# Kernel tuning notes

Measured on AMD Instinct MI355X. Metric: run time of the kernel, lower is better.

Reference implementation:

```python
import jax, jax.numpy as jnp
import numpy as np

BOARD_H, BOARD_W = 10, 9
NUM_NODES = BOARD_H * BOARD_W  # 90
NUM_HEADS = 4


def _build_base_adjacency():
    adj = np.zeros((NUM_NODES, NUM_NODES), dtype=np.float32)
    for y in range(BOARD_H):
        for x in range(BOARD_W):
            idx = y * BOARD_W + x
            for dy, dx in [(0, 1), (0, -1), (1, 0), (-1, 0)]:
                ny, nx = y + dy, x + dx
                if 0 <= ny < BOARD_H and 0 <= nx < BOARD_W:
                    adj[idx, ny * BOARD_W + nx] = 1.0
            for nx in range(BOARD_W):
                if nx != x and abs(nx - x) <= 4:
                    nidx = y * BOARD_W + nx
                    adj[idx, nidx] = max(adj[idx, nidx], 1.0 / abs(nx - x))
            for ny in range(BOARD_H):
                if ny != y and abs(ny - y) <= 5:
                    nidx = ny * BOARD_W + x
                    adj[idx, nidx] = max(adj[idx, nidx], 1.0 / abs(ny - y))
            adj[idx, idx] = 1.0
    deg = np.clip(adj.sum(-1, keepdims=True), 1.0, None)
    return adj / deg  # (90, 90)


def _pos_encoding():
    px = (np.arange(BOARD_W, dtype=np.float32) / BOARD_W)
    py = (np.arange(BOARD_H, dtype=np.float32) / BOARD_H)
    gx = np.broadcast_to(px[None, :], (BOARD_H, BOARD_W)).reshape(-1)
    gy = np.broadcast_to(py[:, None], (BOARD_H, BOARD_W)).reshape(-1)
    return np.stack([gx, gy], axis=-1)  # (90, 2)


def _gat_layer(x, adj, W, a_src, a_dst, gamma, beta):
    B, N, _ = x.shape
    h = (x @ W).reshape(B, N, NUM_HEADS, -1)          # (B,N,H,D)
    s_src = jnp.einsum('bnhd,hd->bhn', h, a_src)       # (B,H,N)
    s_dst = jnp.einsum('bnhd,hd->bhn', h, a_dst)
    attn = s_src[..., :, None] + s_dst[..., None, :]   # (B,H,N,N)
    attn = jax.nn.leaky_relu(attn, 0.2)
    attn = jnp.where((adj == 0)[None, None], -jnp.inf, attn)
    attn = jax.nn.softmax(attn, axis=-1)
    attn = jnp.nan_to_num(attn, nan=0.0)
    out = jnp.einsum('bhij,bjhd->bihd', attn, h).reshape(B * N, -1)
    # BatchNorm1d in training mode: biased batch stats over (B*N)
    mean = out.mean(0)
    var = out.var(0)
    out = (out - mean) * jax.lax.rsqrt(var + 1e-5) * gamma + beta
    return jax.nn.relu(out.reshape(B, N, -1))


def setup_inputs() -> dict:
    key = jax.random.key(0)
    ks = jax.random.split(key, 16)
    B, F_in, Hd, Dout = 2048, 16, 64, 128
    hdim = Hd // NUM_HEADS
    p = lambda k, s: (jax.random.normal(k, s, dtype=jnp.float32) * 0.1)
    return {
        'board_planes': jax.random.uniform(ks[0], (B, 14, BOARD_H, BOARD_W), dtype=jnp.float32),
        'in_W': p(ks[1], (F_in, Hd)), 'in_b': p(ks[2], (Hd,)),
        'W0': p(ks[3], (Hd, Hd)), 'asrc0': p(ks[4], (NUM_HEADS, hdim)), 'adst0': p(ks[5], (NUM_HEADS, hdim)),
        'g0': jnp.ones((Hd,), jnp.float32), 'b0': jnp.zeros((Hd,), jnp.float32),
        'W1': p(ks[6], (Hd, Hd)), 'asrc1': p(ks[7], (NUM_HEADS, hdim)), 'adst1': p(ks[8], (NUM_HEADS, hdim)),
        'g1': jnp.ones((Hd,), jnp.float32), 'b1': jnp.zeros((Hd,), jnp.float32),
        'out_W': p(ks[9], (Hd, Dout)), 'out_b': p(ks[10], (Dout,)),
    }


def reference(board_planes, in_W, in_b, W0, asrc0, adst0, g0, b0,
              W1, asrc1, adst1, g1, b1, out_W, out_b):
    B = board_planes.shape[0]
    adj = jnp.asarray(_build_base_adjacency())            # (90,90), same for all batches
    nodes = board_planes.reshape(B, 14, NUM_NODES).transpose(0, 2, 1)  # (B,90,14)
    pos = jnp.broadcast_to(jnp.asarray(_pos_encoding())[None], (B, NUM_NODES, 2))
    x = jnp.concatenate([nodes, pos], axis=-1)            # (B,90,16)
    x = x @ in_W + in_b
    x = _gat_layer(x, adj, W0, asrc0, adst0, g0, b0)
    x = _gat_layer(x, adj, W1, asrc1, adst1, g1, b1)
    return x.mean(axis=1) @ out_W + out_b                 # (B,128)
```

## Files before the change

### kernel.cpp

```cpp
#include <hip/hip_runtime.h>
#include <cstdint>


#define BB   2048
#define NN   90
#define NP   96
#define CC   64
#define NH   4
#define HD   16
#define TPB  512
#define DOUT 128
#define SXP  72
#define SWP  72
#define PPITCH 20
#define NSLOT 19

typedef _Float16 f16;
typedef _Float16 f16x4 __attribute__((ext_vector_type(4)));
typedef _Float16 f16x8 __attribute__((ext_vector_type(8)));
typedef float f32x4 __attribute__((ext_vector_type(4)));
union U16x4 { f16x4 v; f16 e[4]; };
union U16x8 { f16x8 v; f16 e[8]; };


template <int LAYER>
__global__ __launch_bounds__(TPB, 6) void k_gat(
    const float* __restrict__ bp,
    const float* __restrict__ inW,
    const float* __restrict__ inb,
    const f16*   __restrict__ prevPre,
    const float* __restrict__ stPrev,
    const float* __restrict__ Wl,
    const float* __restrict__ asrc,
    const float* __restrict__ adst,
    f16*   __restrict__ outPre,
    float* __restrict__ partial,
    float* __restrict__ partialSq)
{
    __shared__ __align__(16) unsigned char big[13824];
    __shared__ __align__(16) unsigned char uni[19712];
    __shared__ float sAs[NH * HD], sAd[NH * HD];
    __shared__ float sSrc[NH][NN], sDst[NH][NN];
    __shared__ float sST[2 * CC];

    f16*   sx   = (f16*)big;
    f16*   sh16 = (f16*)big;
    f16*   sWt  = (f16*)uni;
    float* sInW = (float*)(uni + 9216);
    float* sInb = (float*)(uni + 13312);
    float* sXr  = (float*)(uni + 13568);
    f16*   sPh  = (f16*)uni;
    float* sRa  = (float*)uni;
    float* sRb  = (float*)(uni + 8192);

    const int b = blockIdx.x, t = threadIdx.x;
    const int cq = t & 15, ng = t >> 4;
    const int c4 = cq << 2;
    const int jcnt = (ng < NN - 64) ? 3 : 2;
    const int lane = t & 63, wv = t >> 6;
    const int lr = lane & 15, lg = lane >> 4;

    for (int i = t; i < CC * CC; i += TPB) {
        int k = i >> 6, c = i & 63;
        sWt[c * SWP + k] = (f16)Wl[i];
    }
    if (t < NH * HD) { sAs[t] = asrc[t]; sAd[t] = adst[t]; }
    if (t < (NP - NN) * (SXP / 4)) {
        int r = t / (SXP / 4), q = t - r * (SXP / 4);
        f16x4 z = {(f16)0, (f16)0, (f16)0, (f16)0};
        *(f16x4*)&sx[(NN + r) * SXP + q * 4] = z;
    }
    if (LAYER == 0) {
        for (int i = t; i < 16 * CC; i += TPB) sInW[i] = inW[i];
        if (t < CC) sInb[t] = inb[t];
        const float* bpb = bp + (size_t)b * (14 * NN);
        for (int i = t; i < 14 * NN; i += TPB) {
            int p = i / NN, n = i - p * NN;
            sXr[n * 17 + p] = bpb[i];
        }
        if (t < NN) {
            int y = t / 9, x = t - y * 9;
            sXr[t * 17 + 14] = (float)x / 9.0f;
            sXr[t * 17 + 15] = (float)y / 10.0f;
        }
    } else {
        if (t < 2 * CC) sST[t] = stPrev[t];
    }
    __syncthreads();

    if (LAYER == 0) {
        const int n0 = ng, n1 = ng + 32, n2 = (jcnt == 3) ? ng + 64 : ng;
        float acc[3][4] = {};
        #pragma unroll 4
        for (int k = 0; k < 16; k++) {
            float4 w = *(const float4*)&sInW[k * CC + c4];
            float x0 = sXr[n0 * 17 + k], x1 = sXr[n1 * 17 + k], x2 = sXr[n2 * 17 + k];
            acc[0][0] = fmaf(x0, w.x, acc[0][0]); acc[0][1] = fmaf(x0, w.y, acc[0][1]);
            acc[0][2] = fmaf(x0, w.z, acc[0][2]); acc[0][3] = fmaf(x0, w.w, acc[0][3]);
            acc[1][0] = fmaf(x1, w.x, acc[1][0]); acc[1][1] = fmaf(x1, w.y, acc[1][1]);
            acc[1][2] = fmaf(x1, w.z, acc[1][2]); acc[1][3] = fmaf(x1, w.w, acc[1][3]);
            acc[2][0] = fmaf(x2, w.x, acc[2][0]); acc[2][1] = fmaf(x2, w.y, acc[2][1]);
            acc[2][2] = fmaf(x2, w.z, acc[2][2]); acc[2][3] = fmaf(x2, w.w, acc[2][3]);
        }
        float4 bias = *(const float4*)&sInb[c4];
        for (int j = 0; j < jcnt; j++) {
            int n = ng + 32 * j;
            f16x4 o;
            o.x = (f16)(acc[j][0] + bias.x);
            o.y = (f16)(acc[j][1] + bias.y);
            o.z = (f16)(acc[j][2] + bias.z);
            o.w = (f16)(acc[j][3] + bias.w);
            *(f16x4*)&sx[n * SXP + c4] = o;
        }
    } else {
        const f16x8* pv8 = (const f16x8*)(prevPre + (size_t)b * (NN * CC));
        for (int i8 = t; i8 < NN * CC / 8; i8 += TPB) {
            U16x8 v; v.v = pv8[i8];
            int n = i8 >> 3, c8 = (i8 & 7) << 3;
            U16x8 o;
            #pragma unroll
            for (int j = 0; j < 8; j++) {
                float a = fmaf((float)v.e[j], sST[c8 + j], sST[CC + c8 + j]);
                o.e[j] = (f16)(a > 0.0f ? a : 0.0f);
            }
            *(f16x8*)&sx[n * SXP + c8] = o.v;
        }
    }
    __syncthreads();

    {
        const int nt = wv & 3, m0 = wv >> 2;
        const f16x8 bf0 = *(const f16x8*)&sWt[(nt * 16 + lr) * SWP + lg * 8];
        const f16x8 bf1 = *(const f16x8*)&sWt[(nt * 16 + lr) * SWP + 32 + lg * 8];
        f16x8 af0[3], af1[3];
        #pragma unroll
        for (int mi = 0; mi < 3; mi++) {
            const int mt = m0 + 2 * mi;
            af0[mi] = *(const f16x8*)&sx[(mt * 16 + lr) * SXP + lg * 8];
            af1[mi] = *(const f16x8*)&sx[(mt * 16 + lr) * SXP + 32 + lg * 8];
        }
        __syncthreads();
        #pragma unroll
        for (int mi = 0; mi < 3; mi++) {
            const int mt = m0 + 2 * mi;
            f32x4 acc = {0.0f, 0.0f, 0.0f, 0.0f};
            acc = __builtin_amdgcn_mfma_f32_16x16x32_f16(af0[mi], bf0, acc, 0, 0, 0);
            acc = __builtin_amdgcn_mfma_f32_16x16x32_f16(af1[mi], bf1, acc, 0, 0, 0);
            const int row = mt * 16 + lg * 4, col = nt * 16 + lr;
            #pragma unroll
            for (int r = 0; r < 4; r++)
                sh16[(row + r) * SXP + col] = (f16)acc[r];
        }
    }
    __syncthreads();

    if (t < NH * NN) {
        int hh = t / NN, n = t - hh * NN;
        U16x8 h0, h1;
        h0.v = *(const f16x8*)&sh16[n * SXP + hh * HD];
        h1.v = *(const f16x8*)&sh16[n * SXP + hh * HD + 8];
        float a = 0.0f, d = 0.0f;
        #pragma unroll
        for (int j = 0; j < 8; j++) {
            a = fmaf((float)h0.e[j], sAs[hh * HD + j], a);
            a = fmaf((float)h1.e[j], sAs[hh * HD + 8 + j], a);
            d = fmaf((float)h0.e[j], sAd[hh * HD + j], d);
            d = fmaf((float)h1.e[j], sAd[hh * HD + 8 + j], d);
        }
        sSrc[hh][n] = a; sDst[hh][n] = d;
    }
    __syncthreads();

    if (t < NH * NN) {
        int hh = t / NN, n = t - hh * NN;
        int y = n / 9, x = n - y * 9;
        float si = sSrc[hh][n];
        float e[NSLOT];
        #pragma unroll
        for (int xx = 0; xx < 9; xx++) {
            int dx = xx > x ? xx - x : x - xx;
            float ee = si + sDst[hh][y * 9 + xx];
            ee = ee > 0.0f ? ee : 0.2f * ee;
            e[xx] = (dx <= 4) ? ee : -1e30f;
        }
        #pragma unroll
        for (int yy = 0; yy < 10; yy++) {
            int dy = yy > y ? yy - y : y - yy;
            float ee = si + sDst[hh][yy * 9 + x];
            ee = ee > 0.0f ? ee : 0.2f * ee;
            e[9 + yy] = (dy >= 1 && dy <= 5) ? ee : -1e30f;
        }
        float m = e[0];
        #pragma unroll
        for (int k = 1; k < NSLOT; k++) m = fmaxf(m, e[k]);
        float p[NSLOT];
        float s = 0.0f;
        #pragma unroll
        for (int k = 0; k < NSLOT; k++) { p[k] = __expf(e[k] - m); s += p[k]; }
        float inv = 1.0f / s;
        f16* pr = &sPh[t * PPITCH];
        #pragma unroll
        for (int q = 0; q < 5; q++) {
            U16x4 o;
            #pragma unroll
            for (int j = 0; j < 4; j++) {
                int k = 4 * q + j;
                o.e[j] = (k < NSLOT) ? (f16)(p[k] * inv) : (f16)0;
            }
            *(f16x4*)&pr[4 * q] = o.v;
        }
    }
    __syncthreads();

    const int hh2 = cq >> 2;
    float lsum[4] = {}, lsq[4] = {};
    f16* op = outPre + (size_t)b * (NN * CC);
    for (int j = 0; j < jcnt; j++) {
        int n = ng + 32 * j;
        int y = n / 9, x = n - y * 9;
        const f16* pr = &sPh[(hh2 * NN + n) * PPITCH];
        U16x4 P0, P1, P2, P3, P4;
        P0.v = *(const f16x4*)&pr[0];
        P1.v = *(const f16x4*)&pr[4];
        P2.v = *(const f16x4*)&pr[8];
        P3.v = *(const f16x4*)&pr[12];
        P4.v = *(const f16x4*)&pr[16];
        float a0 = 0.0f, a1 = 0.0f, a2 = 0.0f, a3 = 0.0f;
        #pragma unroll
        for (int xx = 0; xx < 9; xx++) {
            float p = (xx < 4) ? (float)P0.e[xx]
                    : (xx < 8) ? (float)P1.e[xx - 4] : (float)P2.e[0];
            U16x4 h4; h4.v = *(const f16x4*)&sh16[(y * 9 + xx) * SXP + c4];
            a0 = fmaf((float)h4.e[0], p, a0); a1 = fmaf((float)h4.e[1], p, a1);
            a2 = fmaf((float)h4.e[2], p, a2); a3 = fmaf((float)h4.e[3], p, a3);
        }
        #pragma unroll
        for (int yy = 0; yy < 10; yy++) {
            int k = 9 + yy;
            float p = (k < 12) ? (float)P2.e[k - 8]
                    : (k < 16) ? (float)P3.e[k - 12] : (float)P4.e[k - 16];
            U16x4 h4; h4.v = *(const f16x4*)&sh16[(yy * 9 + x) * SXP + c4];
            a0 = fmaf((float)h4.e[0], p, a0); a1 = fmaf((float)h4.e[1], p, a1);
            a2 = fmaf((float)h4.e[2], p, a2); a3 = fmaf((float)h4.e[3], p, a3);
        }
        U16x4 o;
        o.e[0] = (f16)a0; o.e[1] = (f16)a1; o.e[2] = (f16)a2; o.e[3] = (f16)a3;
        *(f16x4*)&op[n * CC + c4] = o.v;
        float r0 = (float)o.e[0], r1 = (float)o.e[1];
        float r2 = (float)o.e[2], r3 = (float)o.e[3];
        lsum[0] += r0; lsum[1] += r1; lsum[2] += r2; lsum[3] += r3;
        lsq[0] = fmaf(r0, r0, lsq[0]); lsq[1] = fmaf(r1, r1, lsq[1]);
        lsq[2] = fmaf(r2, r2, lsq[2]); lsq[3] = fmaf(r3, r3, lsq[3]);
    }
    __syncthreads();

    #pragma unroll
    for (int q = 0; q < 4; q++) {
        sRa[ng * CC + c4 + q] = lsum[q];
        sRb[ng * CC + c4 + q] = lsq[q];
    }
    __syncthreads();
    if (t < CC) {
        float s = 0.0f, q2 = 0.0f;
        #pragma unroll
        for (int g = 0; g < 32; g++) {
            s  += sRa[g * CC + t];
            q2 += sRb[g * CC + t];
        }
        partial[(size_t)b * CC + t] = s;
        partialSq[(size_t)b * CC + t] = q2;
    }
}

__global__ __launch_bounds__(256) void k_stats(
    const float* __restrict__ partial, const float* __restrict__ partialSq,
    const float* __restrict__ gamma, const float* __restrict__ beta,
    float* __restrict__ st)
{
    const int c = blockIdx.x, t = threadIdx.x;
    float s = 0.0f, q = 0.0f;
    for (int b = t; b < BB; b += 256) {
        s += partial[(size_t)b * CC + c];
        q += partialSq[(size_t)b * CC + c];
    }
    __shared__ float rs[256], rq[256];
    rs[t] = s; rq[t] = q;
    __syncthreads();
    for (int o = 128; o > 0; o >>= 1) {
        if (t < o) { rs[t] += rs[t + o]; rq[t] += rq[t + o]; }
        __syncthreads();
    }
    if (t == 0) {
        const float cntInv = 1.0f / (float)(BB * NN);
        float mean = rs[0] * cntInv;
        float var  = rq[0] * cntInv - mean * mean;
        float sc = gamma[c] * rsqrtf(var + 1e-5f);
        st[c] = sc;
        st[CC + c] = beta[c] - mean * sc;
    }
}

__global__ __launch_bounds__(256) void k_final(
    const f16* __restrict__ pre, const float* __restrict__ st,
    const float* __restrict__ outW, const float* __restrict__ outb,
    float* __restrict__ out)
{
    __shared__ float sM[CC];
    __shared__ float sPart[4][CC];
    const int b = blockIdx.x, t = threadIdx.x;
    const int c = t & 63, p = t >> 6;
    const f16* pv = pre + (size_t)b * (NN * CC);
    float s = st[c], sft = st[CC + c];
    float a = 0.0f;
    int nBeg = p * 23, nEnd = nBeg + 23 < NN ? nBeg + 23 : NN;
    for (int n = nBeg; n < nEnd; n++) {
        float v = fmaf((float)pv[n * CC + c], s, sft);
        a += (v > 0.0f ? v : 0.0f);
    }
    sPart[p][c] = a;
    __syncthreads();
    if (t < CC)
        sM[t] = (sPart[0][t] + sPart[1][t] + sPart[2][t] + sPart[3][t]) * (1.0f / (float)NN);
    __syncthreads();
    if (t < DOUT) {
        float acc = outb[t];
        #pragma unroll
        for (int cc2 = 0; cc2 < CC; cc2++) acc = fmaf(sM[cc2], outW[cc2 * DOUT + t], acc);
        out[(size_t)b * DOUT + t] = acc;
    }
}

extern "C" void kernel_launch(void* const* d_in, const int* in_sizes, int n_in,
                              void* d_out, int out_size, void* d_ws, size_t ws_size,
                              hipStream_t stream) {
    (void)in_sizes; (void)n_in; (void)out_size; (void)ws_size;

    const float* bp   = (const float*)d_in[0];
    const float* inW  = (const float*)d_in[1];
    const float* inb  = (const float*)d_in[2];
    const float* W0   = (const float*)d_in[3];
    const float* as0  = (const float*)d_in[4];
    const float* ad0  = (const float*)d_in[5];
    const float* g0   = (const float*)d_in[6];
    const float* b0   = (const float*)d_in[7];
    const float* W1   = (const float*)d_in[8];
    const float* as1  = (const float*)d_in[9];
    const float* ad1  = (const float*)d_in[10];
    const float* g1   = (const float*)d_in[11];
    const float* b1   = (const float*)d_in[12];
    const float* outW = (const float*)d_in[13];
    const float* outb = (const float*)d_in[14];
    float* out = (float*)d_out;

    unsigned char* ws = (unsigned char*)d_ws;
    f16*   outPre    = (f16*)ws;
    float* partial   = (float*)(ws + 23592960);
    float* partialSq = (float*)(ws + 23592960 + 524288);
    float* st0       = (float*)(ws + 23592960 + 1048576);
    float* st1       = st0 + 2 * CC;

    k_gat<0><<<BB, TPB, 0, stream>>>(bp, inW, inb, nullptr, nullptr,
                                     W0, as0, ad0, outPre, partial, partialSq);
    k_stats<<<CC, 256, 0, stream>>>(partial, partialSq, g0, b0, st0);
    k_gat<1><<<BB, TPB, 0, stream>>>(nullptr, nullptr, nullptr, outPre, st0,
                                     W1, as1, ad1, outPre, partial, partialSq);
    k_stats<<<CC, 256, 0, stream>>>(partial, partialSq, g1, b1, st1);
    k_final<<<BB, 256, 0, stream>>>(outPre, st1, outW, outb, out);
}
```

Measured before the change: 111.0 us.

## Compute attention scores via MFMA and widen aggregation to 8 channels per thread

Replaces the per-thread scalar dot products for source/destination attention scores with an MFMA against a block-diagonal f16 matrix built from a_src/a_dst. The neighbour aggregation now has each thread handle 8 channels with 16-byte LDS loads instead of 4 channels with 8-byte loads, which halves the number of load instructions. The BatchNorm partial sums are reduced with wave shuffles before a smaller shared-memory reduction. In exchange, the attention coefficients are rounded to f16 inside the MFMA, the thread-to-node mapping leaves some threads idle on the second pass, and the wider accumulators raise register pressure against the occupancy target of 6 set in launch bounds.

```diff
diff --git a/kernel.cpp b/kernel.cpp
--- a/kernel.cpp
+++ b/kernel.cpp
@@ -39,8 +39,8 @@
 {
     __shared__ __align__(16) unsigned char big[13824];
     __shared__ __align__(16) unsigned char uni[19712];
-    __shared__ float sAs[NH * HD], sAd[NH * HD];
     __shared__ float sSrc[NH][NN], sDst[NH][NN];
+    __shared__ __align__(16) f16 sAB[16 * CC];
     __shared__ float sST[2 * CC];
 
     f16*   sx   = (f16*)big;
@@ -64,7 +64,13 @@
         int k = i >> 6, c = i & 63;
         sWt[c * SWP + k] = (f16)Wl[i];
     }
-    if (t < NH * HD) { sAs[t] = asrc[t]; sAd[t] = adst[t]; }
+    for (int i = t; i < 16 * CC; i += TPB) {
+        int c = i >> 6, k = i & 63;
+        float v = 0.0f;
+        if (c < 4)      { if ((k >> 4) == c)     v = asrc[k]; }
+        else if (c < 8) { if ((k >> 4) == c - 4) v = adst[k]; }
+        sAB[i] = (f16)v;
+    }
     if (t < (NP - NN) * (SXP / 4)) {
         int r = t / (SXP / 4), q = t - r * (SXP / 4);
         f16x4 z = {(f16)0, (f16)0, (f16)0, (f16)0};
@@ -154,20 +160,24 @@
     }
     __syncthreads();
 
-    if (t < NH * NN) {
-        int hh = t / NN, n = t - hh * NN;
-        U16x8 h0, h1;
-        h0.v = *(const f16x8*)&sh16[n * SXP + hh * HD];
-        h1.v = *(const f16x8*)&sh16[n * SXP + hh * HD + 8];
-        float a = 0.0f, d = 0.0f;
-        #pragma unroll
-        for (int j = 0; j < 8; j++) {
-            a = fmaf((float)h0.e[j], sAs[hh * HD + j], a);
-            a = fmaf((float)h1.e[j], sAs[hh * HD + 8 + j], a);
-            d = fmaf((float)h0.e[j], sAd[hh * HD + j], d);
-            d = fmaf((float)h1.e[j], sAd[hh * HD + 8 + j], d);
-        }
-        sSrc[hh][n] = a; sDst[hh][n] = d;
+    {
+        const int mt = wv;
+        if (mt < 6) {
+            f16x8 a0 = *(const f16x8*)&sh16[(mt * 16 + lr) * SXP + lg * 8];
+            f16x8 a1 = *(const f16x8*)&sh16[(mt * 16 + lr) * SXP + 32 + lg * 8];
+            f16x8 b0 = *(const f16x8*)&sAB[lr * CC + lg * 8];
+            f16x8 b1 = *(const f16x8*)&sAB[lr * CC + 32 + lg * 8];
+            f32x4 acc = {0.0f, 0.0f, 0.0f, 0.0f};
+            acc = __builtin_amdgcn_mfma_f32_16x16x32_f16(a0, b0, acc, 0, 0, 0);
+            acc = __builtin_amdgcn_mfma_f32_16x16x32_f16(a1, b1, acc, 0, 0, 0);
+            const int row = mt * 16 + lg * 4;
+            if (lr < 8) {
+                float* dstbuf = (lr < 4) ? &sSrc[lr][0] : &sDst[lr - 4][0];
+                #pragma unroll
+                for (int r = 0; r < 4; r++)
+                    if (row + r < NN) dstbuf[row + r] = acc[r];
+            }
+        }
     }
     __syncthreads();
 
@@ -212,60 +222,81 @@
     }
     __syncthreads();
 
-    const int hh2 = cq >> 2;
-    float lsum[4] = {}, lsq[4] = {};
+    const int c8i = t & 7, nr = t >> 3;
+    const int ch = c8i << 3, hh6 = c8i >> 1;
+    float lsum[8] = {}, lsq[8] = {};
     f16* op = outPre + (size_t)b * (NN * CC);
-    for (int j = 0; j < jcnt; j++) {
-        int n = ng + 32 * j;
-        int y = n / 9, x = n - y * 9;
-        const f16* pr = &sPh[(hh2 * NN + n) * PPITCH];
-        U16x4 P0, P1, P2, P3, P4;
-        P0.v = *(const f16x4*)&pr[0];
-        P1.v = *(const f16x4*)&pr[4];
-        P2.v = *(const f16x4*)&pr[8];
-        P3.v = *(const f16x4*)&pr[12];
-        P4.v = *(const f16x4*)&pr[16];
-        float a0 = 0.0f, a1 = 0.0f, a2 = 0.0f, a3 = 0.0f;
-        #pragma unroll
-        for (int xx = 0; xx < 9; xx++) {
-            float p = (xx < 4) ? (float)P0.e[xx]
-                    : (xx < 8) ? (float)P1.e[xx - 4] : (float)P2.e[0];
-            U16x4 h4; h4.v = *(const f16x4*)&sh16[(y * 9 + xx) * SXP + c4];
-            a0 = fmaf((float)h4.e[0], p, a0); a1 = fmaf((float)h4.e[1], p, a1);
-            a2 = fmaf((float)h4.e[2], p, a2); a3 = fmaf((float)h4.e[3], p, a3);
-        }
-        #pragma unroll
-        for (int yy = 0; yy < 10; yy++) {
-            int k = 9 + yy;
-            float p = (k < 12) ? (float)P2.e[k - 8]
-                    : (k < 16) ? (float)P3.e[k - 12] : (float)P4.e[k - 16];
-            U16x4 h4; h4.v = *(const f16x4*)&sh16[(yy * 9 + x) * SXP + c4];
-            a0 = fmaf((float)h4.e[0], p, a0); a1 = fmaf((float)h4.e[1], p, a1);
-            a2 = fmaf((float)h4.e[2], p, a2); a3 = fmaf((float)h4.e[3], p, a3);
-        }
-        U16x4 o;
-        o.e[0] = (f16)a0; o.e[1] = (f16)a1; o.e[2] = (f16)a2; o.e[3] = (f16)a3;
-        *(f16x4*)&op[n * CC + c4] = o.v;
-        float r0 = (float)o.e[0], r1 = (float)o.e[1];
-        float r2 = (float)o.e[2], r3 = (float)o.e[3];
-        lsum[0] += r0; lsum[1] += r1; lsum[2] += r2; lsum[3] += r3;
-        lsq[0] = fmaf(r0, r0, lsq[0]); lsq[1] = fmaf(r1, r1, lsq[1]);
-        lsq[2] = fmaf(r2, r2, lsq[2]); lsq[3] = fmaf(r3, r3, lsq[3]);
-    }
-    __syncthreads();
-
     #pragma unroll
-    for (int q = 0; q < 4; q++) {
-        sRa[ng * CC + c4 + q] = lsum[q];
-        sRb[ng * CC + c4 + q] = lsq[q];
+    for (int j = 0; j < 2; j++) {
+        int n = nr + 64 * j;
+        if (n < NN) {
+            int y = n / 9, x = n - y * 9;
+            const f16* pr = &sPh[(hh6 * NN + n) * PPITCH];
+            U16x4 P0, P1, P2, P3, P4;
+            P0.v = *(const f16x4*)&pr[0];
+            P1.v = *(const f16x4*)&pr[4];
+            P2.v = *(const f16x4*)&pr[8];
+            P3.v = *(const f16x4*)&pr[12];
+            P4.v = *(const f16x4*)&pr[16];
+            float a[8] = {};
+            #pragma unroll
+            for (int xx = 0; xx < 9; xx++) {
+                float p = (xx < 4) ? (float)P0.e[xx]
+                        : (xx < 8) ? (float)P1.e[xx - 4] : (float)P2.e[0];
+                U16x8 h8; h8.v = *(const f16x8*)&sh16[(y * 9 + xx) * SXP + ch];
+                #pragma unroll
+                for (int q = 0; q < 8; q++) a[q] = fmaf((float)h8.e[q], p, a[q]);
+            }
+            #pragma unroll
+            for (int yy = 0; yy < 10; yy++) {
+                int k = 9 + yy;
+                float p = (k < 12) ? (float)P2.e[k - 8]
+                        : (k < 16) ? (float)P3.e[k - 12] : (float)P4.e[k - 16];
+                U16x8 h8; h8.v = *(const f16x8*)&sh16[(yy * 9 + x) * SXP + ch];
+                #pragma unroll
+                for (int q = 0; q < 8; q++) a[q] = fmaf((float)h8.e[q], p, a[q]);
+            }
+            U16x8 o;
+            #pragma unroll
+            for (int q = 0; q < 8; q++) o.e[q] = (f16)a[q];
+            *(f16x8*)&op[n * CC + ch] = o.v;
+            #pragma unroll
+            for (int q = 0; q < 8; q++) {
+                float r = (float)o.e[q];
+                lsum[q] += r;
+                lsq[q] = fmaf(r, r, lsq[q]);
+            }
+        }
+    }
+    __syncthreads();
+
+    #pragma unroll
+    for (int q = 0; q < 8; q++) {
+        float v = lsum[q];
+        v += __shfl_xor(v, 8); v += __shfl_xor(v, 16); v += __shfl_xor(v, 32);
+        lsum[q] = v;
+        float w2 = lsq[q];
+        w2 += __shfl_xor(w2, 8); w2 += __shfl_xor(w2, 16); w2 += __shfl_xor(w2, 32);
+        lsq[q] = w2;
+    }
+    if (lane < 8) {
+        float4 a0, a1, c0, c1;
+        a0.x = lsum[0]; a0.y = lsum[1]; a0.z = lsum[2]; a0.w = lsum[3];
+        a1.x = lsum[4]; a1.y = lsum[5]; a1.z = lsum[6]; a1.w = lsum[7];
+        c0.x = lsq[0];  c0.y = lsq[1];  c0.z = lsq[2];  c0.w = lsq[3];
+        c1.x = lsq[4];  c1.y = lsq[5];  c1.z = lsq[6];  c1.w = lsq[7];
+        *(float4*)&sRa[wv * CC + lane * 8]     = a0;
+        *(float4*)&sRa[wv * CC + lane * 8 + 4] = a1;
+        *(float4*)&sRb[wv * CC + lane * 8]     = c0;
+        *(float4*)&sRb[wv * CC + lane * 8 + 4] = c1;
     }
     __syncthreads();
     if (t < CC) {
         float s = 0.0f, q2 = 0.0f;
         #pragma unroll
-        for (int g = 0; g < 32; g++) {
-            s  += sRa[g * CC + t];
-            q2 += sRb[g * CC + t];
+        for (int w = 0; w < 8; w++) {
+            s  += sRa[w * CC + t];
+            q2 += sRb[w * CC + t];
         }
         partial[(size_t)b * CC + t] = s;
         partialSq[(size_t)b * CC + t] = q2;
```

After: 122.9 us. +10.8%, slower.
